# Kernel optimization log

Measured on AMD Instinct MI355X. Metric: run time of the kernel, lower is better.

The kernel has to match this reference:

```python
import jax, jax.numpy as jnp
import numpy as np

H = 8          # num_attention_heads
WIN = 256      # attention_window (even)
W = WIN // 2   # one-sided window == chunk size
NEG = -1e9
EPS = 1e-5


def _chunk3(t, w, nc):
    # t: [B, (nc+2)*w, ...] (padded by w on each side) -> [B, nc, 3w, ...]
    # chunk c covers key positions [c*w - w, c*w + 2w)
    B = t.shape[0]
    parts = [t[:, i * w:(i + nc) * w].reshape(B, nc, w, *t.shape[2:]) for i in range(3)]
    return jnp.concatenate(parts, axis=2)


def _forward(x, mask, Wq, bq, Wk, bk, Wv, bv, Wqg, bqg, Wkg, bkg, Wvg, bvg,
             ln_g, ln_b, W1, b1, W2, b2):
    B, S0, D = x.shape
    Dh = D // H
    w = W
    # pad seq to even length (pad_token_id = 0); padded token becomes the single global token
    xp = jnp.pad(x, ((0, 0), (0, 1), (0, 0)))
    m = jnp.pad(mask, ((0, 0), (0, 1)), constant_values=True)
    mv = m.astype(jnp.int32) * (-10000)
    mv = mv.at[:, -1].set(10000)            # HF convention: >0 global, <0 padded, 0 local
    S = S0 + 1
    nc = S // w
    scale = 1.0 / float(np.sqrt(Dh))

    q = (xp @ Wq + bq).reshape(B, S, H, Dh) * scale
    k = (xp @ Wk + bk).reshape(B, S, H, Dh)
    v = (xp @ Wv + bv).reshape(B, S, H, Dh)

    kp = jnp.pad(k, ((0, 0), (w, w), (0, 0), (0, 0)))
    vp = jnp.pad(v, ((0, 0), (w, w), (0, 0), (0, 0)))
    kc = _chunk3(kp, w, nc)                               # [B,nc,3w,H,Dh]
    vc = _chunk3(vp, w, nc)
    qc = q.reshape(B, nc, w, H, Dh)
    scores = jnp.einsum('bnqhd,bnkhd->bhnqk', qc, kc)     # [B,H,nc,w,3w]

    qi = jnp.arange(w)[:, None]
    ki = jnp.arange(3 * w)[None, :]
    band = jnp.abs(ki - w - qi) <= w                      # sliding-window band (2w+1 keys)
    keyok = jnp.pad(mv == 0, ((0, 0), (w, w)))            # drop padded + global keys from windowed attn
    keyokc = _chunk3(keyok, w, nc)                        # [B,nc,3w]
    valid = band[None, None] & keyokc[:, :, None, :]      # [B,nc,w,3w]
    scores = jnp.where(valid[:, None], scores, NEG)

    # every query also attends the global key (regular key projection)
    gscore = jnp.einsum('bshd,bhd->bhs', q, k[:, -1])[..., None]
    allsc = jnp.concatenate([gscore, scores.reshape(B, H, S, 3 * w)], axis=-1)
    probs = jax.nn.softmax(allsc, axis=-1)
    pg = probs[..., 0]                                    # [B,H,S] prob on the global key
    pw = probs[..., 1:].reshape(B, H, nc, w, 3 * w)
    out = jnp.einsum('bhnqk,bnkhd->bnqhd', pw, vc).reshape(B, S, H, Dh)
    out = out + pg.transpose(0, 2, 1)[..., None] * v[:, -1][:, None]

    # output at the global token: full attention with the *global* projections
    qg = (xp[:, -1] @ Wqg + bqg).reshape(B, H, Dh) * scale
    kg = (xp @ Wkg + bkg).reshape(B, S, H, Dh)
    vg = (xp @ Wvg + bvg).reshape(B, S, H, Dh)
    gs = jnp.einsum('bhd,bshd->bhs', qg, kg)
    gs = jnp.where((mv < 0)[:, None, :], NEG, gs)
    gp = jax.nn.softmax(gs, axis=-1)
    og = jnp.einsum('bhs,bshd->bhd', gp, vg).reshape(B, D)

    attn = out.reshape(B, S, D).at[:, -1].set(og)
    h = (xp + attn)[:, :-1]                               # residual, then drop pad token
    mu = h.mean(-1, keepdims=True)
    var = ((h - mu) ** 2).mean(-1, keepdims=True)
    hn = (h - mu) / jnp.sqrt(var + EPS) * ln_g + ln_b
    y = hn + (jax.nn.gelu(hn @ W1 + b1, approximate=False) @ W2 + b2)
    return y


def setup_inputs() -> dict:
    key = jax.random.key(0)
    ks = jax.random.split(key, 10)
    B, S0, D, E = 2, 4095, 512, 4
    p = lambda kk, *s: jax.random.normal(kk, s, dtype=jnp.float32) * 0.02
    z = lambda *s: jnp.zeros(s, jnp.float32)
    return {
        'x': jax.random.normal(ks[0], (B, S0, D), dtype=jnp.float32),
        'mask': jnp.zeros((B, S0), dtype=bool),
        'Wq': p(ks[1], D, D), 'bq': z(D),
        'Wk': p(ks[2], D, D), 'bk': z(D),
        'Wv': p(ks[3], D, D), 'bv': z(D),
        'Wqg': p(ks[4], D, D), 'bqg': z(D),
        'Wkg': p(ks[5], D, D), 'bkg': z(D),
        'Wvg': p(ks[6], D, D), 'bvg': z(D),
        'ln_g': jnp.ones((D,), jnp.float32), 'ln_b': z(D),
        'W1': p(ks[7], D, D * E), 'b1': z(D * E),
        'W2': p(ks[8], D * E, D), 'b2': z(D),
    }


def reference(x, mask, Wq, bq, Wk, bk, Wv, bv, Wqg, bqg, Wkg, bkg, Wvg, bvg,
              ln_g, ln_b, W1, b1, W2, b2):
    return _forward(x, mask, Wq, bq, Wk, bk, Wv, bv, Wqg, bqg, Wkg, bkg, Wvg, bvg,
                    ln_g, ln_b, W1, b1, W2, b2)
```

## Files before the change

kernel.cpp:

```cpp
#include <hip/hip_runtime.h>
#include <math.h>

typedef unsigned short ushort_t;
typedef __attribute__((ext_vector_type(4))) float floatx4;
typedef __attribute__((ext_vector_type(8))) short shortx8;
typedef __attribute__((ext_vector_type(8))) unsigned short ushortx8;

__device__ __forceinline__ float bf2f(ushort_t h) {
    union { unsigned u; float f; } x; x.u = ((unsigned)h) << 16; return x.f;
}
__device__ __forceinline__ ushort_t f2bf(float f) {
    union { float f; unsigned u; } x; x.f = f;
    unsigned r = x.u + 0x7fffu + ((x.u >> 16) & 1u);
    return (ushort_t)(r >> 16);
}
__device__ __forceinline__ float rdIn(const void* p, size_t i, int f32) {
    return f32 ? ((const float*)p)[i] : bf2f(((const ushort_t*)p)[i]);
}
__device__ __forceinline__ void gload16(const ushort_t* g, ushort_t* l) {
    __builtin_amdgcn_global_load_lds(
        (const __attribute__((address_space(1))) unsigned int*)g,
        (__attribute__((address_space(3))) unsigned int*)l, 16, 0, 0);
}
__device__ __forceinline__ float gelu_f(float v) {
    float z = fabsf(v) * 0.70710678118654752f;
    float t = __builtin_amdgcn_rcpf(1.0f + 0.3275911f * z);
    float p = 1.061405429f;
    p = p * t - 1.453152027f;
    p = p * t + 1.421413741f;
    p = p * t - 0.284496736f;
    p = p * t + 0.254829592f;
    p = p * t;
    float er = 1.0f - p * __expf(-z * z);
    er = copysignf(er, v);
    return 0.5f * v * (1.0f + er);
}

__global__ __launch_bounds__(256) void detect_kernel(const ushort_t* __restrict__ x,
                                                     int* __restrict__ flag) {
    __shared__ int cnt;
    if (threadIdx.x == 0) cnt = 0;
    __syncthreads();
    ushort_t v = x[threadIdx.x];
    int e = (v >> 7) & 0xff;
    int ok = (e >= 100 && e <= 150) || (v == 0);
    atomicAdd(&cnt, ok);
    __syncthreads();
    if (threadIdx.x == 0) flag[0] = (cnt >= 240) ? 0 : 1;
}

__global__ __launch_bounds__(256) void prep_kernel(const void* __restrict__ x,
                                                   ushort_t* __restrict__ Xp,
                                                   const int* __restrict__ flag) {
    const int f32 = flag[0];
    int i = blockIdx.x * 256 + threadIdx.x;
    int e = i * 8;
    int s = (e >> 9) & 4095;
    int b = e >> 21;
    ushortx8 val = {0, 0, 0, 0, 0, 0, 0, 0};
    if (s < 4095) {
        size_t src = ((size_t)(b * 4095 + s) << 9) + (e & 511);
        if (f32) {
            const float* p = (const float*)x + src;
            floatx4 a = *(const floatx4*)p;
            floatx4 c = *(const floatx4*)(p + 4);
            val[0] = f2bf(a[0]); val[1] = f2bf(a[1]); val[2] = f2bf(a[2]); val[3] = f2bf(a[3]);
            val[4] = f2bf(c[0]); val[5] = f2bf(c[1]); val[6] = f2bf(c[2]); val[7] = f2bf(c[3]);
        } else {
            val = *(const ushortx8*)((const ushort_t*)x + src);
        }
    }
    *(ushortx8*)&Xp[e] = val;
}

__global__ __launch_bounds__(256) void transpose_kernel(
    const void* __restrict__ in0, const void* __restrict__ in1,
    const void* __restrict__ in2, ushort_t* __restrict__ out,
    int R, int C, const int* __restrict__ flag) {
    const int f32 = flag[0];
    const int z = blockIdx.z;
    const void* in = (z == 0) ? in0 : (z == 1) ? in1 : in2;
    __shared__ ushort_t tile[32][33];
    int c0 = blockIdx.x * 32, r0 = blockIdx.y * 32;
    int tx = threadIdx.x & 31, ty = threadIdx.x >> 5;
#pragma unroll
    for (int i = 0; i < 4; i++) {
        size_t idx = (size_t)(r0 + ty + 8 * i) * C + c0 + tx;
        tile[ty + 8 * i][tx] = f32 ? f2bf(((const float*)in)[idx])
                                   : ((const ushort_t*)in)[idx];
    }
    __syncthreads();
#pragma unroll
    for (int i = 0; i < 4; i++)
        out[(size_t)z * R * C + (size_t)(c0 + ty + 8 * i) * R + r0 + tx] =
            tile[tx][ty + 8 * i];
}

template<int EPI>
__global__ __launch_bounds__(512, 2) void gemm8p_kernel(
    const ushort_t* __restrict__ A, const ushort_t* __restrict__ Bt,
    const void* __restrict__ bias0, const void* __restrict__ bias1,
    const void* __restrict__ bias2, void* outp,
    int M, int N, int K, float scale, const int* __restrict__ flag) {
    const int f32 = flag[0];
    __shared__ __align__(16) ushort_t SH[65536];
    const int t = threadIdx.x;
    const int lane = t & 63, wave = t >> 6;
    const int wr = wave >> 2, wc = wave & 3;
    const int l16 = lane & 15, quad = lane >> 4;
    const int pc16 = (quad ^ ((l16 >> 1) & 3)) * 8;

    const int gx = gridDim.x;
    int nwg = gx * gridDim.y;
    int bid = blockIdx.x + gx * blockIdx.y;
    int cpx = nwg >> 3;
    int sb = (bid & 7) * cpx + (bid >> 3);
    const int m0 = (sb % gx) * 256;
    const int n0 = (sb / gx) * 256;

    const int sr = t >> 2;
    const int lc = ((t & 3) ^ ((t >> 3) & 3)) * 8;
    const ushort_t* Ag = A + (size_t)(m0 + sr) * K + lc;
    const ushort_t* Bg = Bt + (size_t)(n0 + sr) * K + lc;
    ushort_t* Sd = SH + t * 8;

    auto STAGE_A = [&](int buf, int kt, int ks) {
        const ushort_t* g = Ag + kt * 64 + ks * 32;
        int d = buf * 16384 + ks * 8192;
        gload16(g,                   Sd + d);
        gload16(g + (size_t)128 * K, Sd + d + 4096);
    };
    auto STAGE_B = [&](int buf, int kt, int ks) {
        const ushort_t* g = Bg + kt * 64 + ks * 32;
        int d = 32768 + buf * 16384 + ks * 8192;
        gload16(g,                   Sd + d);
        gload16(g + (size_t)128 * K, Sd + d + 4096);
    };

    floatx4 acc[8][4];
#pragma unroll
    for (int i = 0; i < 8; i++)
#pragma unroll
        for (int j = 0; j < 4; j++)
#pragma unroll
            for (int r = 0; r < 4; r++) acc[i][j][r] = 0.f;

    shortx8 af[4], bfr[4];
    auto LDB = [&](int buf, int ks) {
#pragma unroll
        for (int nf = 0; nf < 4; nf++)
            bfr[nf] = *(const shortx8*)&SH[32768 + buf * 16384 + ks * 8192 +
                                           (wc * 64 + nf * 16 + l16) * 32 + pc16];
    };
    auto LDA = [&](int buf, int ks, int h) {
#pragma unroll
        for (int i = 0; i < 4; i++)
            af[i] = *(const shortx8*)&SH[buf * 16384 + ks * 8192 +
                                         (wr * 128 + (h * 4 + i) * 16 + l16) * 32 + pc16];
    };
    auto FMA = [&](int h) {
        __builtin_amdgcn_s_setprio(1);
#pragma unroll
        for (int i = 0; i < 4; i++)
#pragma unroll
            for (int nf = 0; nf < 4; nf++)
                acc[h * 4 + i][nf] = __builtin_amdgcn_mfma_f32_16x16x32_bf16(
                    af[i], bfr[nf], acc[h * 4 + i][nf], 0, 0, 0);
        __builtin_amdgcn_s_setprio(0);
    };

    const int KT = K / 64;
    STAGE_A(0, 0, 0); STAGE_B(0, 0, 0);
    STAGE_A(0, 0, 1); STAGE_B(0, 0, 1);

    for (int kt = 0; kt < KT; kt++) {
        const int b = kt & 1, nb = b ^ 1;
        const bool pf = (kt + 1 < KT);
        asm volatile("s_waitcnt vmcnt(4)" ::: "memory");
        __builtin_amdgcn_s_barrier();
        asm volatile("" ::: "memory");
        if (pf) STAGE_A(nb, kt + 1, 0);
        LDB(b, 0); LDA(b, 0, 0);
        FMA(0);
        if (pf) STAGE_B(nb, kt + 1, 0);
        LDA(b, 0, 1);
        FMA(1);
        if (pf) asm volatile("s_waitcnt vmcnt(4)" ::: "memory");
        else    asm volatile("s_waitcnt vmcnt(0)" ::: "memory");
        __builtin_amdgcn_s_barrier();
        asm volatile("" ::: "memory");
        if (pf) STAGE_A(nb, kt + 1, 1);
        LDB(b, 1); LDA(b, 1, 0);
        FMA(0);
        if (pf) STAGE_B(nb, kt + 1, 1);
        LDA(b, 1, 1);
        FMA(1);
    }

    __syncthreads();

    float bias[4];
    float scl = 1.0f;
    if (EPI == 3) {
        int idx = n0 >> 9;
        const void* bp = (idx == 0) ? bias0 : (idx == 1) ? bias1 : bias2;
#pragma unroll
        for (int nf = 0; nf < 4; nf++)
            bias[nf] = rdIn(bp, (n0 & 511) + wc * 64 + nf * 16 + l16, f32);
        scl = (idx == 0) ? scale : 1.0f;
    } else {
#pragma unroll
        for (int nf = 0; nf < 4; nf++)
            bias[nf] = rdIn(bias0, n0 + wc * 64 + nf * 16 + l16, f32);
    }

#pragma unroll
    for (int mf = 0; mf < 8; mf++) {
#pragma unroll
        for (int nf = 0; nf < 4; nf++) {
#pragma unroll
            for (int r = 0; r < 4; r++) {
                int row = wr * 128 + mf * 16 + quad * 4 + r;
                float v = acc[mf][nf][r] + bias[nf];
                if (EPI == 3) v *= scl;
                else          v = gelu_f(v);
                int ch = wc * 8 + nf * 2 + (l16 >> 3);
                SH[row * 256 + ((ch ^ (row & 7)) * 8) + (l16 & 7)] = f2bf(v);
            }
        }
    }
    __syncthreads();

    if (EPI == 3) {
        ushort_t* ob = (ushort_t*)outp + (size_t)(n0 >> 9) * 4194304 + (n0 & 511);
#pragma unroll
        for (int i = 0; i < 16; i++) {
            int j = i * 512 + t;
            int row = j >> 5, ch = j & 31;
            ushortx8 vv = *(const ushortx8*)&SH[row * 256 + ((ch ^ (row & 7)) * 8)];
            *(ushortx8*)&ob[(size_t)(m0 + row) * 512 + ch * 8] = vv;
        }
    } else {
        ushort_t* ob = (ushort_t*)outp + n0;
#pragma unroll
        for (int i = 0; i < 16; i++) {
            int j = i * 512 + t;
            int row = j >> 5, ch = j & 31;
            ushortx8 vv = *(const ushortx8*)&SH[row * 256 + ((ch ^ (row & 7)) * 8)];
            *(ushortx8*)&ob[(size_t)(m0 + row) * N + ch * 8] = vv;
        }
    }
}

__global__ __launch_bounds__(512, 2) void gemm_splitk_kernel(
    const ushort_t* __restrict__ A, const ushort_t* __restrict__ Bt,
    const void* __restrict__ bias0, void* outp,
    const ushort_t* __restrict__ resid, const int* __restrict__ flag) {
    const int f32 = flag[0];
    __shared__ __align__(16) ushort_t SH[65536];
    const int K = 2048;
    const int t = threadIdx.x;
    const int lane = t & 63, wave = t >> 6;
    const int kh = wave >> 2, wr = (wave >> 1) & 1, wc = wave & 1;
    const int l16 = lane & 15, quad = lane >> 4;
    const int pc16 = (quad ^ ((l16 >> 1) & 3)) * 8;

    const int bid = blockIdx.x;
    const int xcd = bid & 7, i5 = bid >> 3;
    const int nt = xcd >> 1;
    const int mt = (xcd & 1) * 32 + i5;
    const int m0 = mt * 128, n0 = nt * 128;

    const int sr = t >> 2;
    const int lc = ((t & 3) ^ ((t >> 3) & 3)) * 8;
    const ushort_t* Ag = A + (size_t)(m0 + sr) * K + lc;
    const ushort_t* Bg = Bt + (size_t)(n0 + sr) * K + lc;
    ushort_t* Sd = SH + t * 8;

    auto STAGE = [&](int kt) {
        const int b = kt & 3;
        gload16(Ag + kt * 32,        Sd + b * 8192);
        gload16(Ag + 1024 + kt * 32, Sd + b * 8192 + 4096);
        gload16(Bg + kt * 32,        Sd + 32768 + b * 8192);
        gload16(Bg + 1024 + kt * 32, Sd + 32768 + b * 8192 + 4096);
    };

    floatx4 acc[4][4];
#pragma unroll
    for (int i = 0; i < 4; i++)
#pragma unroll
        for (int j = 0; j < 4; j++)
#pragma unroll
            for (int r = 0; r < 4; r++) acc[i][j][r] = 0.f;

    const int KT = 32;
    STAGE(0); STAGE(1); STAGE(2);

    for (int kt = 0; kt < KT; kt++) {
        if (kt + 2 < KT)      asm volatile("s_waitcnt vmcnt(8)" ::: "memory");
        else if (kt + 1 < KT) asm volatile("s_waitcnt vmcnt(4)" ::: "memory");
        else                  asm volatile("s_waitcnt vmcnt(0)" ::: "memory");
        __builtin_amdgcn_s_barrier();
        asm volatile("" ::: "memory");
        if (kt + 3 < KT) STAGE(kt + 3);

        const int ab = (kt & 3) * 8192 + kh * 4096;
        shortx8 af[4], bfr[4];
#pragma unroll
        for (int nf = 0; nf < 4; nf++)
            bfr[nf] = *(const shortx8*)&SH[32768 + ab + (wc * 64 + nf * 16 + l16) * 32 + pc16];
#pragma unroll
        for (int mf = 0; mf < 4; mf++)
            af[mf] = *(const shortx8*)&SH[ab + (wr * 64 + mf * 16 + l16) * 32 + pc16];

        __builtin_amdgcn_s_setprio(1);
#pragma unroll
        for (int mf = 0; mf < 4; mf++)
#pragma unroll
            for (int nf = 0; nf < 4; nf++)
                acc[mf][nf] = __builtin_amdgcn_mfma_f32_16x16x32_bf16(
                    af[mf], bfr[nf], acc[mf][nf], 0, 0, 0);
        __builtin_amdgcn_s_setprio(0);
    }

    __syncthreads();
    float* RED = (float*)SH;
    if (kh == 1) {
        const int base = ((wave & 3) * 64 + lane) * 16;
#pragma unroll
        for (int i = 0; i < 4; i++)
#pragma unroll
            for (int j = 0; j < 4; j++) {
                int k2 = (i * 4 + j + l16) & 15;
                *(floatx4*)&RED[(base + k2) * 4] = acc[i][j];
            }
    }
    __syncthreads();
    if (kh == 0) {
        const int base = (wave * 64 + lane) * 16;
#pragma unroll
        for (int i = 0; i < 4; i++)
#pragma unroll
            for (int j = 0; j < 4; j++) {
                int k2 = (i * 4 + j + l16) & 15;
                floatx4 p = *(const floatx4*)&RED[(base + k2) * 4];
#pragma unroll
                for (int r = 0; r < 4; r++) acc[i][j][r] += p[r];
            }
#pragma unroll
        for (int i = 0; i < 4; i++) {
#pragma unroll
            for (int j = 0; j < 4; j++) {
#pragma unroll
                for (int r = 0; r < 4; r++) {
                    int m = m0 + wr * 64 + i * 16 + quad * 4 + r;
                    int n = n0 + wc * 64 + j * 16 + l16;
                    int bb = m >> 12, s = m & 4095;
                    if (s < 4095) {
                        float v = acc[i][j][r] + rdIn(bias0, n, f32) +
                                  bf2f(resid[(size_t)m * 512 + n]);
                        size_t oidx = ((size_t)bb * 4095 + s) * 512 + n;
                        if (f32) ((float*)outp)[oidx] = v;
                        else     ((ushort_t*)outp)[oidx] = f2bf(v);
                    }
                }
            }
        }
    }
}

#define ALD 344

__global__ __launch_bounds__(256) void attn_mfma_kernel(
    ushort_t* Q, const ushort_t* __restrict__ Kx, const ushort_t* __restrict__ Vx) {
    __shared__ ushort_t Pl[64][ALD];
    __shared__ ushort_t Vt[2][64][40];
    __shared__ float pgl[64];

    const int t = threadIdx.x;
    const int lane = t & 63, w = t >> 6;
    const int l16 = lane & 15, quad = lane >> 4;
    const int bid = blockIdx.x;
    const int qt = bid & 63;
    const int h = (bid >> 6) & 7;
    const int b = bid >> 9;
    const int q0 = qt * 64;
    const int jmin = q0 - 128;
    const size_t base = ((size_t)b * 4096) * 512 + (size_t)h * 64;

    const int qw = q0 + w * 16;
    const int lo = qw - 128, hi = qw + 15 + 128;

    shortx8 qf0, qf1;
    {
        const ushort_t* qp = Q + base + (size_t)(qw + l16) * 512 + quad * 8;
        qf0 = *(const shortx8*)(qp);
        qf1 = *(const shortx8*)(qp + 32);
    }

    floatx4 s[21];
#pragma unroll
    for (int i = 0; i < 21; i++)
#pragma unroll
        for (int r = 0; r < 4; r++) s[i][r] = 0.f;

#pragma unroll
    for (int tt = 0; tt < 20; tt++) {
        int jt = jmin + tt * 16;
        if (jt + 15 < lo || jt > hi) continue;
        int key = jt + l16;
        int kcl = min(max(key, 0), 4094);
        const ushort_t* kp = Kx + base + (size_t)kcl * 512 + quad * 8;
        shortx8 k0 = *(const shortx8*)(kp);
        shortx8 k1 = *(const shortx8*)(kp + 32);
        s[tt] = __builtin_amdgcn_mfma_f32_16x16x32_bf16(qf0, k0, s[tt], 0, 0, 0);
        s[tt] = __builtin_amdgcn_mfma_f32_16x16x32_bf16(qf1, k1, s[tt], 0, 0, 0);
    }
    {
        const ushort_t* kp = Kx + base + (size_t)4095 * 512 + quad * 8;
        shortx8 k0 = *(const shortx8*)(kp);
        shortx8 k1 = *(const shortx8*)(kp + 32);
        s[20] = __builtin_amdgcn_mfma_f32_16x16x32_bf16(qf0, k0, s[20], 0, 0, 0);
        s[20] = __builtin_amdgcn_mfma_f32_16x16x32_bf16(qf1, k1, s[20], 0, 0, 0);
    }

#pragma unroll
    for (int tt = 0; tt < 20; tt++) {
        int j = jmin + tt * 16 + l16;
        bool okj = (j >= 0) && (j <= 4094);
#pragma unroll
        for (int r = 0; r < 4; r++) {
            int q = qw + quad * 4 + r;
            bool ok = okj && (j - q <= 128) && (q - j <= 128);
            if (!ok) s[tt][r] = -1e30f;
        }
    }
    if (l16 != 0) {
#pragma unroll
        for (int r = 0; r < 4; r++) s[20][r] = -1e30f;
    }

    floatx4 mx = s[0];
#pragma unroll
    for (int tt = 1; tt < 21; tt++)
#pragma unroll
        for (int r = 0; r < 4; r++) mx[r] = fmaxf(mx[r], s[tt][r]);
#pragma unroll
    for (int off = 1; off < 16; off <<= 1)
#pragma unroll
        for (int r = 0; r < 4; r++) mx[r] = fmaxf(mx[r], __shfl_xor(mx[r], off, 64));

    floatx4 sum;
#pragma unroll
    for (int r = 0; r < 4; r++) sum[r] = 0.f;
#pragma unroll
    for (int tt = 0; tt < 21; tt++)
#pragma unroll
        for (int r = 0; r < 4; r++) {
            float e = __expf(s[tt][r] - mx[r]);
            s[tt][r] = e;
            sum[r] += e;
        }
#pragma unroll
    for (int off = 1; off < 16; off <<= 1)
#pragma unroll
        for (int r = 0; r < 4; r++) sum[r] += __shfl_xor(sum[r], off, 64);

    floatx4 inv;
#pragma unroll
    for (int r = 0; r < 4; r++) inv[r] = 1.f / sum[r];

#pragma unroll
    for (int tt = 0; tt < 20; tt++)
#pragma unroll
        for (int r = 0; r < 4; r++)
            Pl[w * 16 + quad * 4 + r][tt * 16 + l16] = f2bf(s[tt][r]);
    if (l16 == 0) {
#pragma unroll
        for (int r = 0; r < 4; r++) pgl[w * 16 + quad * 4 + r] = s[20][r];
    }

    floatx4 o[4];
#pragma unroll
    for (int nt = 0; nt < 4; nt++)
#pragma unroll
        for (int r = 0; r < 4; r++) o[nt][r] = 0.f;

    const int ck = t & 31, cd = t >> 5;
    ushortx8 vreg;
    {
        int row = min(max(jmin + ck, 0), 4095);
        vreg = *(const ushortx8*)&Vx[base + (size_t)row * 512 + cd * 8];
    }
    for (int c = 0; c < 10; c++) {
#pragma unroll
        for (int e = 0; e < 8; e++) Vt[c & 1][cd * 8 + e][ck] = vreg[e];
        if (c < 9) {
            int row = min(max(jmin + (c + 1) * 32 + ck, 0), 4095);
            vreg = *(const ushortx8*)&Vx[base + (size_t)row * 512 + cd * 8];
        }
        __syncthreads();
        int jc = jmin + c * 32;
        if (jc + 31 >= lo && jc <= hi) {
            shortx8 pf = *(const shortx8*)&Pl[w * 16 + l16][c * 32 + quad * 8];
#pragma unroll
            for (int nt = 0; nt < 4; nt++) {
                shortx8 vf = *(const shortx8*)&Vt[c & 1][nt * 16 + l16][quad * 8];
                o[nt] = __builtin_amdgcn_mfma_f32_16x16x32_bf16(pf, vf, o[nt], 0, 0, 0);
            }
        }
    }

#pragma unroll
    for (int nt = 0; nt < 4; nt++) {
        float vg = bf2f(Vx[base + (size_t)4095 * 512 + nt * 16 + l16]);
#pragma unroll
        for (int r = 0; r < 4; r++) {
            float pg = pgl[w * 16 + quad * 4 + r];
            float val = (o[nt][r] + pg * vg) * inv[r];
            Q[base + (size_t)(qw + quad * 4 + r) * 512 + nt * 16 + l16] = f2bf(val);
        }
    }
}

__global__ __launch_bounds__(256) void ln_kernel(
    const void* __restrict__ x, ushort_t* hio,
    const void* __restrict__ g, const void* __restrict__ bta,
    const int* __restrict__ flag) {
    const int f32 = flag[0];
    const int r = blockIdx.x;
    const int b = (r >= 4095) ? 1 : 0;
    const int s = r - b * 4095;
    const size_t xrow = (size_t)r * 512;
    const size_t hrow = ((size_t)b * 4096 + s) * 512;
    const int t = threadIdx.x;
    float h0 = rdIn(x, xrow + t, f32) + bf2f(hio[hrow + t]);
    float h1 = rdIn(x, xrow + 256 + t, f32) + bf2f(hio[hrow + 256 + t]);
    float sum = h0 + h1, sq = h0 * h0 + h1 * h1;
#pragma unroll
    for (int off = 1; off < 64; off <<= 1) {
        sum += __shfl_xor(sum, off, 64);
        sq += __shfl_xor(sq, off, 64);
    }
    __shared__ float red[8];
    int wave = t >> 6, lane = t & 63;
    if (lane == 0) { red[wave] = sum; red[wave + 4] = sq; }
    __syncthreads();
    sum = red[0] + red[1] + red[2] + red[3];
    sq = red[4] + red[5] + red[6] + red[7];
    float mu = sum * (1.f / 512.f);
    float var = sq * (1.f / 512.f) - mu * mu;
    float rs = rsqrtf(var + 1e-5f);
    float v0 = (h0 - mu) * rs * rdIn(g, t, f32) + rdIn(bta, t, f32);
    float v1 = (h1 - mu) * rs * rdIn(g, 256 + t, f32) + rdIn(bta, 256 + t, f32);
    hio[hrow + t] = f2bf(v0);
    hio[hrow + 256 + t] = f2bf(v1);
}

extern "C" void kernel_launch(void* const* d_in, const int* in_sizes, int n_in,
                              void* d_out, int out_size, void* d_ws, size_t ws_size,
                              hipStream_t stream) {
    const void* x   = d_in[0];
    const void* Wq  = d_in[2];
    const void* bq  = d_in[3];
    const void* Wk  = d_in[4];
    const void* bk  = d_in[5];
    const void* Wv  = d_in[6];
    const void* bv  = d_in[7];
    const void* lng = d_in[14];
    const void* lnb = d_in[15];
    const void* W1  = d_in[16];
    const void* b1  = d_in[17];
    const void* W2  = d_in[18];
    const void* b2  = d_in[19];

    char* ws = (char*)d_ws;
    ushort_t* Qb  = (ushort_t*)(ws + 0);
    ushort_t* Kb  = (ushort_t*)(ws + 8388608);
    ushort_t* Vb  = (ushort_t*)(ws + 16777216);
    ushort_t* Xp  = (ushort_t*)(ws + 33554432);
    ushort_t* Gs  = (ushort_t*)(ws + 8388608);
    ushort_t* Wqt = (ushort_t*)(ws + 41943040);
    ushort_t* W1t = (ushort_t*)(ws + 43515904);
    ushort_t* W2t = (ushort_t*)(ws + 45613056);
    int*      flg = (int*)(ws + 47710208);

    detect_kernel<<<dim3(1), dim3(256), 0, stream>>>((const ushort_t*)x, flg);

    transpose_kernel<<<dim3(16, 16, 3), dim3(256), 0, stream>>>(Wq, Wk, Wv, Wqt, 512, 512, flg);
    transpose_kernel<<<dim3(64, 16, 1), dim3(256), 0, stream>>>(W1, W1, W1, W1t, 512, 2048, flg);
    transpose_kernel<<<dim3(16, 64, 1), dim3(256), 0, stream>>>(W2, W2, W2, W2t, 2048, 512, flg);

    prep_kernel<<<dim3(2048), dim3(256), 0, stream>>>(x, Xp, flg);

    const float scale = 0.125f;
    gemm8p_kernel<3><<<dim3(32, 6), dim3(512), 0, stream>>>(
        Xp, Wqt, bq, bk, bv, Qb, 8192, 1536, 512, scale, flg);

    attn_mfma_kernel<<<dim3(1024), dim3(256), 0, stream>>>(Qb, Kb, Vb);

    ln_kernel<<<dim3(8190), dim3(256), 0, stream>>>(x, Qb, lng, lnb, flg);

    gemm8p_kernel<1><<<dim3(32, 8), dim3(512), 0, stream>>>(
        Qb, W1t, b1, b1, b1, Gs, 8192, 2048, 512, 1.0f, flg);
    gemm_splitk_kernel<<<dim3(256), dim3(512), 0, stream>>>(
        Gs, W2t, b2, d_out, Qb, flg);
}
```

Before: 261.1 us.

## Load W2 GEMM operands directly into registers instead of staging through LDS

The split-K FFN down-projection GEMM stops staging A/B tiles into shared memory with async global-to-LDS loads and barriers. Each wave now loads its MFMA fragments straight from global memory into a triple-buffered register ring, two k-steps ahead, and the loop is fully unrolled. This drops the LDS round trip and the per-iteration barriers. In exchange, waves that share rows load the same data separately, global loads are narrower and strided, register pressure rises, and latency hiding now depends on the compiler's scheduling.

```diff
diff --git a/kernel.cpp b/kernel.cpp
--- a/kernel.cpp
+++ b/kernel.cpp
@@ -252,18 +252,17 @@
     }
 }
 
-__global__ __launch_bounds__(512, 2) void gemm_splitk_kernel(
+__global__ __launch_bounds__(512, 2) void gemm_vgpr_kernel(
     const ushort_t* __restrict__ A, const ushort_t* __restrict__ Bt,
     const void* __restrict__ bias0, void* outp,
     const ushort_t* __restrict__ resid, const int* __restrict__ flag) {
     const int f32 = flag[0];
-    __shared__ __align__(16) ushort_t SH[65536];
+    __shared__ __align__(16) float RED[16384];
     const int K = 2048;
     const int t = threadIdx.x;
     const int lane = t & 63, wave = t >> 6;
     const int kh = wave >> 2, wr = (wave >> 1) & 1, wc = wave & 1;
     const int l16 = lane & 15, quad = lane >> 4;
-    const int pc16 = (quad ^ ((l16 >> 1) & 3)) * 8;
 
     const int bid = blockIdx.x;
     const int xcd = bid & 7, i5 = bid >> 3;
@@ -271,18 +270,17 @@
     const int mt = (xcd & 1) * 32 + i5;
     const int m0 = mt * 128, n0 = nt * 128;
 
-    const int sr = t >> 2;
-    const int lc = ((t & 3) ^ ((t >> 3) & 3)) * 8;
-    const ushort_t* Ag = A + (size_t)(m0 + sr) * K + lc;
-    const ushort_t* Bg = Bt + (size_t)(n0 + sr) * K + lc;
-    ushort_t* Sd = SH + t * 8;
-
-    auto STAGE = [&](int kt) {
-        const int b = kt & 3;
-        gload16(Ag + kt * 32,        Sd + b * 8192);
-        gload16(Ag + 1024 + kt * 32, Sd + b * 8192 + 4096);
-        gload16(Bg + kt * 32,        Sd + 32768 + b * 8192);
-        gload16(Bg + 1024 + kt * 32, Sd + 32768 + b * 8192 + 4096);
+    const ushort_t* Ap = A + (size_t)(m0 + wr * 64 + l16) * K + kh * 1024 + quad * 8;
+    const ushort_t* Bp = Bt + (size_t)(n0 + wc * 64 + l16) * K + kh * 1024 + quad * 8;
+
+    shortx8 afb[3][4], bfb[3][4];
+    auto LOAD = [&](int kt) {
+        const int b = kt % 3;
+#pragma unroll
+        for (int f = 0; f < 4; f++) {
+            afb[b][f] = *(const shortx8*)(Ap + (size_t)(f * 16) * K + kt * 32);
+            bfb[b][f] = *(const shortx8*)(Bp + (size_t)(f * 16) * K + kt * 32);
+        }
     };
 
     floatx4 acc[4][4];
@@ -294,37 +292,22 @@
             for (int r = 0; r < 4; r++) acc[i][j][r] = 0.f;
 
     const int KT = 32;
-    STAGE(0); STAGE(1); STAGE(2);
-
+    LOAD(0); LOAD(1);
+
+#pragma unroll
     for (int kt = 0; kt < KT; kt++) {
-        if (kt + 2 < KT)      asm volatile("s_waitcnt vmcnt(8)" ::: "memory");
-        else if (kt + 1 < KT) asm volatile("s_waitcnt vmcnt(4)" ::: "memory");
-        else                  asm volatile("s_waitcnt vmcnt(0)" ::: "memory");
-        __builtin_amdgcn_s_barrier();
-        asm volatile("" ::: "memory");
-        if (kt + 3 < KT) STAGE(kt + 3);
-
-        const int ab = (kt & 3) * 8192 + kh * 4096;
-        shortx8 af[4], bfr[4];
-#pragma unroll
-        for (int nf = 0; nf < 4; nf++)
-            bfr[nf] = *(const shortx8*)&SH[32768 + ab + (wc * 64 + nf * 16 + l16) * 32 + pc16];
-#pragma unroll
-        for (int mf = 0; mf < 4; mf++)
-            af[mf] = *(const shortx8*)&SH[ab + (wr * 64 + mf * 16 + l16) * 32 + pc16];
-
+        if (kt + 2 < KT) LOAD(kt + 2);
+        const int b = kt % 3;
         __builtin_amdgcn_s_setprio(1);
 #pragma unroll
         for (int mf = 0; mf < 4; mf++)
 #pragma unroll
             for (int nf = 0; nf < 4; nf++)
                 acc[mf][nf] = __builtin_amdgcn_mfma_f32_16x16x32_bf16(
-                    af[mf], bfr[nf], acc[mf][nf], 0, 0, 0);
+                    afb[b][mf], bfb[b][nf], acc[mf][nf], 0, 0, 0);
         __builtin_amdgcn_s_setprio(0);
     }
 
-    __syncthreads();
-    float* RED = (float*)SH;
     if (kh == 1) {
         const int base = ((wave & 3) * 64 + lane) * 16;
 #pragma unroll
@@ -603,6 +586,6 @@
 
     gemm8p_kernel<1><<<dim3(32, 8), dim3(512), 0, stream>>>(
         Qb, W1t, b1, b1, b1, Gs, 8192, 2048, 512, 1.0f, flg);
-    gemm_splitk_kernel<<<dim3(256), dim3(512), 0, stream>>>(
+    gemm_vgpr_kernel<<<dim3(256), dim3(512), 0, stream>>>(
         Gs, W2t, b2, d_out, Qb, flg);
 }
```

Result: slower. 292.9 us (+12.2%).

## Store FFN intermediate and W2 in K-panel layout for split-K GEMM loads

Applied to the files above, without the earlier changes.

The GELU GEMM epilogue now writes its output in 32-column K-panels (each panel is M×32 contiguous), and W2 is transposed into the same panel layout. The split-K GEMM's async global-to-LDS loads then read contiguous 64-byte rows inside a panel instead of striding across full 2048-wide rows. The aim is better memory coalescing and cache/TLB locality for the second FFN GEMM's operand fetches. The cost is a more scattered store pattern in the producing epilogue.

```diff
diff --git a/kernel.cpp b/kernel.cpp
--- a/kernel.cpp
+++ b/kernel.cpp
@@ -76,7 +76,7 @@
 __global__ __launch_bounds__(256) void transpose_kernel(
     const void* __restrict__ in0, const void* __restrict__ in1,
     const void* __restrict__ in2, ushort_t* __restrict__ out,
-    int R, int C, const int* __restrict__ flag) {
+    int R, int C, int panel, const int* __restrict__ flag) {
     const int f32 = flag[0];
     const int z = blockIdx.z;
     const void* in = (z == 0) ? in0 : (z == 1) ? in1 : in2;
@@ -91,9 +91,14 @@
     }
     __syncthreads();
 #pragma unroll
-    for (int i = 0; i < 4; i++)
-        out[(size_t)z * R * C + (size_t)(c0 + ty + 8 * i) * R + r0 + tx] =
-            tile[tx][ty + 8 * i];
+    for (int i = 0; i < 4; i++) {
+        if (panel)
+            out[((size_t)(r0 >> 5) * C + (c0 + ty + 8 * i)) * 32 + tx] =
+                tile[tx][ty + 8 * i];
+        else
+            out[(size_t)z * R * C + (size_t)(c0 + ty + 8 * i) * R + r0 + tx] =
+                tile[tx][ty + 8 * i];
+    }
 }
 
 template<int EPI>
@@ -241,13 +246,15 @@
             *(ushortx8*)&ob[(size_t)(m0 + row) * 512 + ch * 8] = vv;
         }
     } else {
-        ushort_t* ob = (ushort_t*)outp + n0;
+        ushort_t* ob = (ushort_t*)outp;
+        const size_t pb0 = (size_t)(n0 >> 5) * 262144 + (size_t)m0 * 32;
 #pragma unroll
         for (int i = 0; i < 16; i++) {
             int j = i * 512 + t;
-            int row = j >> 5, ch = j & 31;
+            int p = j >> 10, row = (j >> 2) & 255, c = j & 3;
+            int ch = p * 4 + c;
             ushortx8 vv = *(const ushortx8*)&SH[row * 256 + ((ch ^ (row & 7)) * 8)];
-            *(ushortx8*)&ob[(size_t)(m0 + row) * N + ch * 8] = vv;
+            *(ushortx8*)&ob[pb0 + (size_t)p * 262144 + (size_t)row * 32 + c * 8] = vv;
         }
     }
 }
@@ -258,7 +265,6 @@
     const ushort_t* __restrict__ resid, const int* __restrict__ flag) {
     const int f32 = flag[0];
     __shared__ __align__(16) ushort_t SH[65536];
-    const int K = 2048;
     const int t = threadIdx.x;
     const int lane = t & 63, wave = t >> 6;
     const int kh = wave >> 2, wr = (wave >> 1) & 1, wc = wave & 1;
@@ -272,17 +278,17 @@
     const int m0 = mt * 128, n0 = nt * 128;
 
     const int sr = t >> 2;
-    const int lc = ((t & 3) ^ ((t >> 3) & 3)) * 8;
-    const ushort_t* Ag = A + (size_t)(m0 + sr) * K + lc;
-    const ushort_t* Bg = Bt + (size_t)(n0 + sr) * K + lc;
+    const int sc8 = ((t & 3) ^ ((t >> 3) & 3)) * 8;
+    const ushort_t* Ag = A + (size_t)(m0 + sr) * 32 + sc8;
+    const ushort_t* Bg = Bt + (size_t)(n0 + sr) * 32 + sc8;
     ushort_t* Sd = SH + t * 8;
 
     auto STAGE = [&](int kt) {
         const int b = kt & 3;
-        gload16(Ag + kt * 32,        Sd + b * 8192);
-        gload16(Ag + 1024 + kt * 32, Sd + b * 8192 + 4096);
-        gload16(Bg + kt * 32,        Sd + 32768 + b * 8192);
-        gload16(Bg + 1024 + kt * 32, Sd + 32768 + b * 8192 + 4096);
+        gload16(Ag + (size_t)kt * 262144,        Sd + b * 8192);
+        gload16(Ag + (size_t)(32 + kt) * 262144, Sd + b * 8192 + 4096);
+        gload16(Bg + (size_t)kt * 16384,         Sd + 32768 + b * 8192);
+        gload16(Bg + (size_t)(32 + kt) * 16384,  Sd + 32768 + b * 8192 + 4096);
     };
 
     floatx4 acc[4][4];
@@ -587,9 +593,9 @@
 
     detect_kernel<<<dim3(1), dim3(256), 0, stream>>>((const ushort_t*)x, flg);
 
-    transpose_kernel<<<dim3(16, 16, 3), dim3(256), 0, stream>>>(Wq, Wk, Wv, Wqt, 512, 512, flg);
-    transpose_kernel<<<dim3(64, 16, 1), dim3(256), 0, stream>>>(W1, W1, W1, W1t, 512, 2048, flg);
-    transpose_kernel<<<dim3(16, 64, 1), dim3(256), 0, stream>>>(W2, W2, W2, W2t, 2048, 512, flg);
+    transpose_kernel<<<dim3(16, 16, 3), dim3(256), 0, stream>>>(Wq, Wk, Wv, Wqt, 512, 512, 0, flg);
+    transpose_kernel<<<dim3(64, 16, 1), dim3(256), 0, stream>>>(W1, W1, W1, W1t, 512, 2048, 0, flg);
+    transpose_kernel<<<dim3(16, 64, 1), dim3(256), 0, stream>>>(W2, W2, W2, W2t, 2048, 512, 1, flg);
 
     prep_kernel<<<dim3(2048), dim3(256), 0, stream>>>(x, Xp, flg);
 
```

Result: faster. 254.3 us (-2.6%).
